# Performance work log

Hardware: AMD Instinct MI355X
Metric: run time of the kernel (lower is better)

The kernel has to match this reference:

```python
import jax, jax.numpy as jnp
import numpy as np

N_NODES = 50000
N_EDGES = 800000
N_GRAPHS = 64
IN_CH = 128
HID = 128
PROC_X = 128
Q_DIM = 768
PROC_Q = 128
OUT_CH = 32


def setup_inputs() -> dict:
    key = jax.random.key(0)
    ks = jax.random.split(key, 16)
    inp = {
        "x": jax.random.normal(ks[0], (N_NODES, IN_CH), dtype=jnp.float32),
        "edge_index": jax.random.randint(ks[1], (2, N_EDGES), 0, N_NODES, dtype=jnp.int64),
        "batch": jnp.sort(jax.random.randint(ks[2], (N_NODES,), 0, N_GRAPHS, dtype=jnp.int64)),
        "question_embedding": jax.random.normal(ks[3], (N_GRAPHS, Q_DIM), dtype=jnp.float32),
    }
    s = 1.0 / np.sqrt(HID)
    inp["W0"] = jax.random.uniform(ks[4], (IN_CH, HID), minval=-s, maxval=s)
    inp["b0"] = jnp.zeros((HID,), jnp.float32)
    inp["W1"] = jax.random.uniform(ks[5], (HID, HID), minval=-s, maxval=s)
    inp["b1"] = jnp.zeros((HID,), jnp.float32)
    inp["W2"] = jax.random.uniform(ks[6], (HID, PROC_X), minval=-s, maxval=s)
    inp["b2"] = jnp.zeros((PROC_X,), jnp.float32)
    inp["fc0_w"] = jax.random.uniform(ks[7], (Q_DIM, PROC_Q), minval=-s, maxval=s)
    inp["fc0_b"] = jnp.zeros((PROC_Q,), jnp.float32)
    inp["fc1_w"] = jax.random.uniform(ks[8], (PROC_X + PROC_Q, HID), minval=-s, maxval=s)
    inp["fc1_b"] = jnp.zeros((HID,), jnp.float32)
    inp["fc2_w"] = jax.random.uniform(ks[9], (HID, OUT_CH), minval=-s, maxval=s)
    inp["fc2_b"] = jnp.zeros((OUT_CH,), jnp.float32)
    return inp


def _gcn_norm(edge_index, n_nodes):
    """Add self-loops and compute symmetric GCN normalization per edge."""
    loop = jnp.arange(n_nodes, dtype=edge_index.dtype)
    src = jnp.concatenate([edge_index[0], loop])
    dst = jnp.concatenate([edge_index[1], loop])
    ones = jnp.ones_like(dst, dtype=jnp.float32)
    deg = jax.ops.segment_sum(ones, dst, num_segments=n_nodes)
    dinv = jnp.where(deg > 0, jax.lax.rsqrt(deg), 0.0)
    norm = dinv[src] * dinv[dst]  # [E+N]
    return src, dst, norm


def _gcn_conv(x, src, dst, norm, W, b):
    h = x @ W                                # [N, F_out]
    msg = h[src] * norm[:, None]             # gather + scale  [E+N, F_out]
    agg = jax.ops.segment_sum(msg, dst, num_segments=x.shape[0])
    return agg + b


def reference(x, edge_index, batch, question_embedding,
              W0, b0, W1, b1, W2, b2,
              fc0_w, fc0_b, fc1_w, fc1_b, fc2_w, fc2_b):
    n = x.shape[0]
    src, dst, norm = _gcn_norm(edge_index, n)
    h = jax.nn.relu(_gcn_conv(x, src, dst, norm, W0, b0))
    h = jax.nn.relu(_gcn_conv(h, src, dst, norm, W1, b1))
    h = jax.nn.relu(_gcn_conv(h, src, dst, norm, W2, b2))
    q = jax.nn.relu(question_embedding @ fc0_w + fc0_b)  # [G, PROC_Q]
    q_exp = q[batch]                                      # [N, PROC_Q]
    combined = jnp.concatenate([h, q_exp], axis=1)
    out = jax.nn.relu(combined @ fc1_w + fc1_b)
    out = out @ fc2_w + fc2_b
    return out
```

## Files before the change

### kernel.cpp

```cpp
#include <hip/hip_runtime.h>
#include <hip/hip_bf16.h>

#define N_NODES 50000
#define N_EDGES 800000
#define N_GRAPHS 64
#define LSTR 136

typedef __attribute__((ext_vector_type(4))) short s4v;
typedef __attribute__((ext_vector_type(8))) short s8v;
typedef __attribute__((ext_vector_type(16))) float f16v;

struct HL { short hi, lo; };

__device__ inline HL bsplit(float f) {
    HL r;
    unsigned u = __float_as_uint(f);
    unsigned rh = (u + 0x7FFFu + ((u >> 16) & 1u)) >> 16;
    r.hi = (short)rh;
    float fh = __uint_as_float(rh << 16);
    float fl = f - fh;
    unsigned u2 = __float_as_uint(fl);
    unsigned rl = (u2 + 0x7FFFu + ((u2 >> 16) & 1u)) >> 16;
    r.lo = (short)rl;
    return r;
}

__device__ inline unsigned short f2bf(float f) {
    unsigned u = __float_as_uint(f);
    return (unsigned short)((u + 0x7FFFu + ((u >> 16) & 1u)) >> 16);
}

__device__ inline float bflo(unsigned u) { return __uint_as_float(u << 16); }
__device__ inline float bfhi(unsigned u) { return __uint_as_float(u & 0xFFFF0000u); }


__global__ void k_hist(const int* __restrict__ ei, int* __restrict__ cnt,
                       int* __restrict__ rank, int E) {
    int e = blockIdx.x * 256 + threadIdx.x;
    if (e < E) rank[e] = atomicAdd(&cnt[ei[E + e]], 1);
}

__global__ __launch_bounds__(512) void k_scan_a(const int* __restrict__ cnt,
                                                int* __restrict__ rowptr,
                                                int* __restrict__ bsum,
                                                float* __restrict__ dinv, int n) {
    __shared__ int s[512];
    int t = threadIdx.x;
    int i = blockIdx.x * 512 + t;
    int v = (i < n) ? cnt[i] : 0;
    if (i < n) dinv[i] = rsqrtf((float)(v + 1));
    int pv = (v + 7) & ~7;
    s[t] = pv;
    __syncthreads();
    for (int d = 1; d < 512; d <<= 1) {
        int x = (t >= d) ? s[t - d] : 0;
        __syncthreads();
        s[t] += x;
        __syncthreads();
    }
    if (i < n) rowptr[i] = s[t] - pv;
    if (t == 511) bsum[blockIdx.x] = s[511];
}

__global__ __launch_bounds__(512) void k_scan_c(int* __restrict__ rowptr,
                                                const int* __restrict__ bsum,
                                                int n, int nb) {
    __shared__ int sb[128];
    int t = threadIdx.x;
    if (t < 128) sb[t] = (t < nb) ? bsum[t] : 0;
    __syncthreads();
    for (int d = 1; d < 128; d <<= 1) {
        int x = 0;
        if (t < 128 && t >= d) x = sb[t - d];
        __syncthreads();
        if (t < 128) sb[t] += x;
        __syncthreads();
    }
    int add = (blockIdx.x > 0) ? sb[blockIdx.x - 1] : 0;
    int i = blockIdx.x * 512 + t;
    if (i < n) rowptr[i] += add;
    if (i == 0) rowptr[n] = sb[nb - 1];
}

__global__ void k_fill_csr(const int* __restrict__ ei, const int* __restrict__ rowptr,
                           const int* __restrict__ rank,
                           unsigned short* __restrict__ colA, int E) {
    int e = blockIdx.x * 256 + threadIdx.x;
    if (e >= E) return;
    colA[rowptr[ei[E + e]] + rank[e]] = (unsigned short)ei[e];
}

__global__ __launch_bounds__(512) void k_prep(const float* __restrict__ qe,
                                              const float* __restrict__ fc0w,
                                              const float* __restrict__ fc0b,
                                              const float* __restrict__ fc1w,
                                              const float* __restrict__ fc1b,
                                              const float* __restrict__ W0,
                                              const float* __restrict__ W1,
                                              const float* __restrict__ W2,
                                              const float* __restrict__ fc2w,
                                              short* __restrict__ WH,
                                              short* __restrict__ WL,
                                              int* __restrict__ cntz,
                                              unsigned* __restrict__ Hsd,
                                              unsigned* __restrict__ Hsd2,
                                              unsigned short* __restrict__ colA,
                                              float* __restrict__ qq) {
    int b = blockIdx.x, tid = threadIdx.x;
    if (b >= 225) {
        int idx = (b - 225) * 512 + tid;
        if (idx < 143752) {
            uint4 p;
            p.x = p.y = p.z = p.w = 0xC350C350u;
            ((uint4*)colA)[idx] = p;
        }
        return;
    }
    if (b >= 200) {
        int idx = (b - 200) * 512 + tid;
        if (idx < 12504) ((int4*)cntz)[idx] = make_int4(0, 0, 0, 0);
        if (b == 200 && tid < 64) {
            Hsd[(unsigned)N_NODES * 64u + tid] = 0u;
            Hsd2[(unsigned)N_NODES * 64u + tid] = 0u;
        }
        return;
    }
    if (b >= 64) {
        int i = (b - 64) * 512 + tid;
        float val;
        int dst;
        if (i < 65536) {
            int mat = i >> 14, off = i & 16383;
            int k = off >> 7, n = off & 127;
            const float* src = (mat == 0) ? W0 : (mat == 1) ? W1 : (mat == 2) ? W2 : fc1w;
            val = src[k * 128 + n];
            dst = mat * 16384 + n * 128 + k;
        } else {
            int off = i - 65536;
            int k = off >> 5, n = off & 31;
            val = fc2w[k * 32 + n];
            dst = 65536 + n * 128 + k;
        }
        HL r = bsplit(val);
        WH[dst] = r.hi;
        WL[dst] = r.lo;
        return;
    }
    __shared__ float qs[768];
    __shared__ float red[512];
    __shared__ float ql[128];
    const float* fc1bot = fc1w + 128 * 128;
    int g = b;
    for (int i = tid; i < 768; i += 512) qs[i] = qe[g * 768 + i];
    __syncthreads();
    int j = tid & 127, sl = tid >> 7;
    int kb = sl * 192;
    float a0 = 0, a1 = 0, a2 = 0, a3 = 0;
    for (int k = 0; k < 192; k += 4) {
        a0 += qs[kb + k + 0] * fc0w[(kb + k + 0) * 128 + j];
        a1 += qs[kb + k + 1] * fc0w[(kb + k + 1) * 128 + j];
        a2 += qs[kb + k + 2] * fc0w[(kb + k + 2) * 128 + j];
        a3 += qs[kb + k + 3] * fc0w[(kb + k + 3) * 128 + j];
    }
    red[tid] = (a0 + a1) + (a2 + a3);
    __syncthreads();
    if (tid < 128)
        ql[tid] = fmaxf(((red[tid] + red[tid + 128]) + (red[tid + 256] + red[tid + 384]))
                        + fc0b[tid], 0.f);
    __syncthreads();
    kb = sl * 32;
    float b0 = 0, b1 = 0;
    for (int k = 0; k < 32; k += 2) {
        b0 += ql[kb + k + 0] * fc1bot[(kb + k + 0) * 128 + j];
        b1 += ql[kb + k + 1] * fc1bot[(kb + k + 1) * 128 + j];
    }
    red[tid] = b0 + b1;
    __syncthreads();
    if (tid < 128)
        qq[g * 128 + tid] = ((red[tid] + red[tid + 128]) + (red[tid + 256] + red[tid + 384]))
                            + fc1b[tid];
}

__global__ __launch_bounds__(128) void gemm_mf(const float* __restrict__ A32,
                                               const short* __restrict__ WTh,
                                               const short* __restrict__ WTl,
                                               const float* __restrict__ dinv,
                                               unsigned short* __restrict__ oHs,
                                               int nrows) {
    __shared__ short Ah[32 * LSTR];
    const int tid = threadIdx.x;
    const int row0 = blockIdx.x * 32;

    #pragma unroll
    for (int i = 0; i < 8; ++i) {
        int u = i * 128 + tid;
        int r = u >> 5, c4 = u & 31;
        int gr = row0 + r;
        float4 v = make_float4(0.f, 0.f, 0.f, 0.f);
        if (gr < nrows) v = ((const float4*)A32)[(size_t)gr * 32 + c4];
        s4v h4 = {(short)f2bf(v.x), (short)f2bf(v.y), (short)f2bf(v.z), (short)f2bf(v.w)};
        *(s4v*)&Ah[r * LSTR + c4 * 4] = h4;
    }
    __syncthreads();

    const int wv = tid >> 6, lane = tid & 63;
    const int m = lane & 31, half = lane >> 5;
    const int c0 = wv * 64 + m;
    f16v acc0 = {0.f}, acc1 = {0.f};
    #pragma unroll
    for (int ks = 0; ks < 8; ++ks) {
        int ko = ks * 16 + half * 8;
        s8v ah  = *(const s8v*)&Ah[m * LSTR + ko];
        s8v bh0 = *(const s8v*)&WTh[(size_t)c0 * 128 + ko];
        s8v bl0 = *(const s8v*)&WTl[(size_t)c0 * 128 + ko];
        s8v bh1 = *(const s8v*)&WTh[(size_t)(c0 + 32) * 128 + ko];
        s8v bl1 = *(const s8v*)&WTl[(size_t)(c0 + 32) * 128 + ko];
        acc0 = __builtin_amdgcn_mfma_f32_32x32x16_bf16(ah, bh0, acc0, 0, 0, 0);
        acc0 = __builtin_amdgcn_mfma_f32_32x32x16_bf16(ah, bl0, acc0, 0, 0, 0);
        acc1 = __builtin_amdgcn_mfma_f32_32x32x16_bf16(ah, bh1, acc1, 0, 0, 0);
        acc1 = __builtin_amdgcn_mfma_f32_32x32x16_bf16(ah, bl1, acc1, 0, 0, 0);
    }

    #pragma unroll
    for (int reg = 0; reg < 16; ++reg) {
        int rl = (reg & 3) + 8 * (reg >> 2) + 4 * half;
        int gr = row0 + rl;
        if (gr >= nrows) continue;
        float sc = dinv[gr];
        oHs[(size_t)gr * 128 + c0]      = f2bf(acc0[reg] * sc);
        oHs[(size_t)gr * 128 + c0 + 32] = f2bf(acc1[reg] * sc);
    }
}

template <int FC>
__global__ __launch_bounds__(256) void k_gg(const unsigned* __restrict__ Hs,
                                            const int* __restrict__ rowptr,
                                            const unsigned short* __restrict__ colA,
                                            const float* __restrict__ dinv,
                                            const float* __restrict__ bias,
                                            const short* __restrict__ WTh,
                                            const short* __restrict__ WTl,
                                            const short* __restrict__ W2h,
                                            const short* __restrict__ W2l,
                                            const float* __restrict__ qq,
                                            const int* __restrict__ batch,
                                            const float* __restrict__ fc2b,
                                            unsigned short* __restrict__ oHs,
                                            float* __restrict__ out,
                                            int n) {
    __shared__ short Ah[32 * LSTR];
    __shared__ short Pl[FC ? 32 * LSTR : 1];
    __shared__ float red[FC ? 3 * 32 * 33 : 1];
    const int tid = threadIdx.x;
    const int row0 = blockIdx.x * 32;
    const int wv = tid >> 6, l = tid & 63;
    const int m = l & 31, half = l >> 5;

    const float2 bb = ((const float2*)bias)[l];
    for (int i = 0; i < 8; ++i) {
        int r = wv * 8 + i;
        int node = row0 + r;
        unsigned pack = 0;
        if (node < n) {
            int e0 = __builtin_amdgcn_readfirstlane(rowptr[node]);
            int e1 = __builtin_amdgcn_readfirstlane(rowptr[node + 1]);
            float a0 = 0.f, a1 = 0.f;
            for (int e = e0; e < e1; e += 8) {
                uint4 cw = *(const uint4*)(colA + e);
                unsigned u0 = Hs[(cw.x & 0xFFFFu) * 64u + l];
                unsigned u1 = Hs[(cw.x >> 16) * 64u + l];
                unsigned u2 = Hs[(cw.y & 0xFFFFu) * 64u + l];
                unsigned u3 = Hs[(cw.y >> 16) * 64u + l];
                unsigned u4 = Hs[(cw.z & 0xFFFFu) * 64u + l];
                unsigned u5 = Hs[(cw.z >> 16) * 64u + l];
                unsigned u6 = Hs[(cw.w & 0xFFFFu) * 64u + l];
                unsigned u7 = Hs[(cw.w >> 16) * 64u + l];
                a0 += ((bflo(u0) + bflo(u1)) + (bflo(u2) + bflo(u3)))
                    + ((bflo(u4) + bflo(u5)) + (bflo(u6) + bflo(u7)));
                a1 += ((bfhi(u0) + bfhi(u1)) + (bfhi(u2) + bfhi(u3)))
                    + ((bfhi(u4) + bfhi(u5)) + (bfhi(u6) + bfhi(u7)));
            }
            float di = dinv[node];
            unsigned uh = Hs[(unsigned)node * 64u + l];
            float o0 = fmaxf((a0 + bflo(uh)) * di + bb.x, 0.f);
            float o1 = fmaxf((a1 + bfhi(uh)) * di + bb.y, 0.f);
            pack = (unsigned)f2bf(o0) | ((unsigned)f2bf(o1) << 16);
        }
        ((unsigned*)Ah)[r * 68 + l] = pack;
    }
    __syncthreads();

    const int c0 = wv * 32 + m;
    f16v acc = {0.f};
    #pragma unroll
    for (int ks = 0; ks < 8; ++ks) {
        int ko = ks * 16 + half * 8;
        s8v ah = *(const s8v*)&Ah[m * LSTR + ko];
        s8v bh = *(const s8v*)&WTh[(size_t)c0 * 128 + ko];
        s8v bl = *(const s8v*)&WTl[(size_t)c0 * 128 + ko];
        acc = __builtin_amdgcn_mfma_f32_32x32x16_bf16(ah, bh, acc, 0, 0, 0);
        acc = __builtin_amdgcn_mfma_f32_32x32x16_bf16(ah, bl, acc, 0, 0, 0);
    }

    if (FC == 0) {
        #pragma unroll
        for (int reg = 0; reg < 16; ++reg) {
            int rl = (reg & 3) + 8 * (reg >> 2) + 4 * half;
            int gr = row0 + rl;
            if (gr >= n) continue;
            oHs[(size_t)gr * 128 + c0] = f2bf(acc[reg] * dinv[gr]);
        }
    } else {
        __syncthreads();
        #pragma unroll
        for (int reg = 0; reg < 16; ++reg) {
            int rl = (reg & 3) + 8 * (reg >> 2) + 4 * half;
            int gr = row0 + rl;
            int g = (gr < n) ? batch[gr] : 0;
            float v = fmaxf(acc[reg] + qq[(size_t)g * 128 + c0], 0.f);
            HL p = bsplit(v);
            Ah[rl * LSTR + c0] = p.hi;
            Pl[rl * LSTR + c0] = p.lo;
        }
        __syncthreads();
        f16v acc2 = {0.f};
        #pragma unroll
        for (int ks = 0; ks < 2; ++ks) {
            int ko = wv * 32 + ks * 16 + half * 8;
            s8v ah = *(const s8v*)&Ah[m * LSTR + ko];
            s8v al = *(const s8v*)&Pl[m * LSTR + ko];
            s8v bh = *(const s8v*)&W2h[(size_t)m * 128 + ko];
            s8v bl = *(const s8v*)&W2l[(size_t)m * 128 + ko];
            acc2 = __builtin_amdgcn_mfma_f32_32x32x16_bf16(ah, bh, acc2, 0, 0, 0);
            acc2 = __builtin_amdgcn_mfma_f32_32x32x16_bf16(ah, bl, acc2, 0, 0, 0);
            acc2 = __builtin_amdgcn_mfma_f32_32x32x16_bf16(al, bh, acc2, 0, 0, 0);
        }
        if (wv > 0) {
            #pragma unroll
            for (int reg = 0; reg < 16; ++reg) {
                int rl = (reg & 3) + 8 * (reg >> 2) + 4 * half;
                red[(wv - 1) * 1056 + rl * 33 + m] = acc2[reg];
            }
        }
        __syncthreads();
        if (wv == 0) {
            #pragma unroll
            for (int reg = 0; reg < 16; ++reg) {
                int rl = (reg & 3) + 8 * (reg >> 2) + 4 * half;
                int gr = row0 + rl;
                if (gr < n)
                    out[(size_t)gr * 32 + m] = acc2[reg]
                        + (red[rl * 33 + m] + red[1056 + rl * 33 + m])
                        + red[2112 + rl * 33 + m] + fc2b[m];
            }
        }
    }
}


extern "C" void kernel_launch(void* const* d_in, const int* in_sizes, int n_in,
                              void* d_out, int out_size, void* d_ws, size_t ws_size,
                              hipStream_t stream) {
    const float* x    = (const float*)d_in[0];
    const int*   ei   = (const int*)d_in[1];
    const int*   batch= (const int*)d_in[2];
    const float* qe   = (const float*)d_in[3];
    const float* W0   = (const float*)d_in[4];
    const float* b0   = (const float*)d_in[5];
    const float* W1   = (const float*)d_in[6];
    const float* b1   = (const float*)d_in[7];
    const float* W2   = (const float*)d_in[8];
    const float* b2   = (const float*)d_in[9];
    const float* fc0w = (const float*)d_in[10];
    const float* fc0b = (const float*)d_in[11];
    const float* fc1w = (const float*)d_in[12];
    const float* fc1b = (const float*)d_in[13];
    const float* fc2w = (const float*)d_in[14];
    const float* fc2b = (const float*)d_in[15];
    float* out = (float*)d_out;

    float* WS = (float*)d_ws;
    unsigned short* HS  = (unsigned short*)WS;
    unsigned short* HS2 = (unsigned short*)(WS + 3200064);
    float* DINV = WS + 6400128;
    float* QQ   = WS + 6450144;
    int*   CNT  = (int*)(WS + 6458336);
    int*   ROWPTR = (int*)(WS + 6508352);
    int*   RANK = (int*)(WS + 6558368);
    unsigned short* COL = (unsigned short*)(WS + 7358368);
    int*   BSUM = (int*)(WS + 7933376);
    short* WTH  = (short*)(WS + 7933504);
    short* WTL  = WTH + 69632;

    const int N = N_NODES, E = N_EDGES;
    const int eb = (E + 255) / 256;
    const int sb = (N + 511) / 512;
    const int gg = (N + 31) / 32;

    k_prep<<<506, 512, 0, stream>>>(qe, fc0w, fc0b, fc1w, fc1b, W0, W1, W2, fc2w,
                                    WTH, WTL, CNT, (unsigned*)HS, (unsigned*)HS2, COL, QQ);
    k_hist<<<eb, 256, 0, stream>>>(ei, CNT, RANK, E);
    k_scan_a<<<sb, 512, 0, stream>>>(CNT, ROWPTR, BSUM, DINV, N);
    k_scan_c<<<sb, 512, 0, stream>>>(ROWPTR, BSUM, N, sb);
    k_fill_csr<<<eb, 256, 0, stream>>>(ei, ROWPTR, RANK, COL, E);

    gemm_mf<<<gg, 128, 0, stream>>>(x, WTH, WTL, DINV, HS, N);
    k_gg<0><<<gg, 256, 0, stream>>>((const unsigned*)HS, ROWPTR, COL, DINV, b0,
                                    WTH + 16384, WTL + 16384, nullptr, nullptr,
                                    nullptr, nullptr, nullptr, HS2, nullptr, N);
    k_gg<0><<<gg, 256, 0, stream>>>((const unsigned*)HS2, ROWPTR, COL, DINV, b1,
                                    WTH + 32768, WTL + 32768, nullptr, nullptr,
                                    nullptr, nullptr, nullptr, HS, nullptr, N);
    k_gg<1><<<gg, 256, 0, stream>>>((const unsigned*)HS, ROWPTR, COL, DINV, b2,
                                    WTH + 49152, WTL + 49152, WTH + 65536, WTL + 65536,
                                    QQ, batch, fc2b, nullptr, out, N);
}
```

Baseline: 323.1 us.

## Fuse CSR build into one cooperative kernel and interleave two-row gathers

Four separate CSR-construction kernels (histogram, two scan passes, fill) are merged into one cooperative kernel of 512 blocks that uses grid-wide syncs between phases, removing launch gaps. Separately, the aggregation loop in the GCN layer kernel now processes two destination rows at once, interleaving their gathers to raise memory-level parallelism. The cooperative launch requires all 512 blocks to be co-resident and adds grid-sync costs. The paired loop adds extra registers and tail loops when the two rows have unequal degree.

```diff
diff --git a/kernel.cpp b/kernel.cpp
--- a/kernel.cpp
+++ b/kernel.cpp
@@ -1,5 +1,8 @@
 #include <hip/hip_runtime.h>
 #include <hip/hip_bf16.h>
+#include <hip/hip_cooperative_groups.h>
+
+namespace cg = cooperative_groups;
 
 #define N_NODES 50000
 #define N_EDGES 800000
@@ -33,61 +36,81 @@
 __device__ inline float bflo(unsigned u) { return __uint_as_float(u << 16); }
 __device__ inline float bfhi(unsigned u) { return __uint_as_float(u & 0xFFFF0000u); }
 
-
-__global__ void k_hist(const int* __restrict__ ei, int* __restrict__ cnt,
-                       int* __restrict__ rank, int E) {
-    int e = blockIdx.x * 256 + threadIdx.x;
-    if (e < E) rank[e] = atomicAdd(&cnt[ei[E + e]], 1);
-}
-
-__global__ __launch_bounds__(512) void k_scan_a(const int* __restrict__ cnt,
-                                                int* __restrict__ rowptr,
-                                                int* __restrict__ bsum,
-                                                float* __restrict__ dinv, int n) {
+__device__ inline void gat8(const unsigned* __restrict__ Hs,
+                            const unsigned short* __restrict__ colA,
+                            int e, int l, float& a0, float& a1) {
+    uint4 cw = *(const uint4*)(colA + e);
+    unsigned u0 = Hs[(cw.x & 0xFFFFu) * 64u + l];
+    unsigned u1 = Hs[(cw.x >> 16) * 64u + l];
+    unsigned u2 = Hs[(cw.y & 0xFFFFu) * 64u + l];
+    unsigned u3 = Hs[(cw.y >> 16) * 64u + l];
+    unsigned u4 = Hs[(cw.z & 0xFFFFu) * 64u + l];
+    unsigned u5 = Hs[(cw.z >> 16) * 64u + l];
+    unsigned u6 = Hs[(cw.w & 0xFFFFu) * 64u + l];
+    unsigned u7 = Hs[(cw.w >> 16) * 64u + l];
+    a0 += ((bflo(u0) + bflo(u1)) + (bflo(u2) + bflo(u3)))
+        + ((bflo(u4) + bflo(u5)) + (bflo(u6) + bflo(u7)));
+    a1 += ((bfhi(u0) + bfhi(u1)) + (bfhi(u2) + bfhi(u3)))
+        + ((bfhi(u4) + bfhi(u5)) + (bfhi(u6) + bfhi(u7)));
+}
+
+__global__ __launch_bounds__(512) void k_csr(const int* __restrict__ ei,
+                                             int* __restrict__ cnt,
+                                             int* __restrict__ rank,
+                                             int* __restrict__ rowptr,
+                                             int* __restrict__ bsum,
+                                             float* __restrict__ dinv,
+                                             unsigned short* __restrict__ colA,
+                                             int n, int E) {
+    cg::grid_group grid = cg::this_grid();
+    const int t = threadIdx.x;
+    const int gid = blockIdx.x * 512 + t;
+    const int gsz = gridDim.x * 512;
+    const int nb = (n + 511) / 512;
+
+    for (int e = gid; e < E; e += gsz)
+        rank[e] = atomicAdd(&cnt[ei[E + e]], 1);
+    grid.sync();
+
     __shared__ int s[512];
-    int t = threadIdx.x;
-    int i = blockIdx.x * 512 + t;
-    int v = (i < n) ? cnt[i] : 0;
-    if (i < n) dinv[i] = rsqrtf((float)(v + 1));
-    int pv = (v + 7) & ~7;
-    s[t] = pv;
-    __syncthreads();
-    for (int d = 1; d < 512; d <<= 1) {
-        int x = (t >= d) ? s[t - d] : 0;
+    __shared__ int sb[128];
+    if (blockIdx.x < nb) {
+        int i = blockIdx.x * 512 + t;
+        int v = (i < n) ? cnt[i] : 0;
+        if (i < n) dinv[i] = rsqrtf((float)(v + 1));
+        int pv = (v + 7) & ~7;
+        s[t] = pv;
         __syncthreads();
-        s[t] += x;
+        for (int d = 1; d < 512; d <<= 1) {
+            int x = (t >= d) ? s[t - d] : 0;
+            __syncthreads();
+            s[t] += x;
+            __syncthreads();
+        }
+        if (i < n) rowptr[i] = s[t] - pv;
+        if (t == 511) bsum[blockIdx.x] = s[511];
+    }
+    grid.sync();
+
+    if (blockIdx.x < nb) {
+        if (t < 128) sb[t] = (t < nb) ? bsum[t] : 0;
         __syncthreads();
-    }
-    if (i < n) rowptr[i] = s[t] - pv;
-    if (t == 511) bsum[blockIdx.x] = s[511];
-}
-
-__global__ __launch_bounds__(512) void k_scan_c(int* __restrict__ rowptr,
-                                                const int* __restrict__ bsum,
-                                                int n, int nb) {
-    __shared__ int sb[128];
-    int t = threadIdx.x;
-    if (t < 128) sb[t] = (t < nb) ? bsum[t] : 0;
-    __syncthreads();
-    for (int d = 1; d < 128; d <<= 1) {
-        int x = 0;
-        if (t < 128 && t >= d) x = sb[t - d];
-        __syncthreads();
-        if (t < 128) sb[t] += x;
-        __syncthreads();
-    }
-    int add = (blockIdx.x > 0) ? sb[blockIdx.x - 1] : 0;
-    int i = blockIdx.x * 512 + t;
-    if (i < n) rowptr[i] += add;
-    if (i == 0) rowptr[n] = sb[nb - 1];
-}
-
-__global__ void k_fill_csr(const int* __restrict__ ei, const int* __restrict__ rowptr,
-                           const int* __restrict__ rank,
-                           unsigned short* __restrict__ colA, int E) {
-    int e = blockIdx.x * 256 + threadIdx.x;
-    if (e >= E) return;
-    colA[rowptr[ei[E + e]] + rank[e]] = (unsigned short)ei[e];
+        for (int d = 1; d < 128; d <<= 1) {
+            int x = 0;
+            if (t < 128 && t >= d) x = sb[t - d];
+            __syncthreads();
+            if (t < 128) sb[t] += x;
+            __syncthreads();
+        }
+        int add = (blockIdx.x > 0) ? sb[blockIdx.x - 1] : 0;
+        int i = blockIdx.x * 512 + t;
+        if (i < n) rowptr[i] += add;
+        if (i == 0) rowptr[n] = sb[nb - 1];
+    }
+    grid.sync();
+
+    for (int e = gid; e < E; e += gsz)
+        colA[rowptr[ei[E + e]] + rank[e]] = (unsigned short)ei[e];
 }
 
 __global__ __launch_bounds__(512) void k_prep(const float* __restrict__ qe,
@@ -257,36 +280,45 @@
     const int m = l & 31, half = l >> 5;
 
     const float2 bb = ((const float2*)bias)[l];
-    for (int i = 0; i < 8; ++i) {
-        int r = wv * 8 + i;
-        int node = row0 + r;
-        unsigned pack = 0;
-        if (node < n) {
-            int e0 = __builtin_amdgcn_readfirstlane(rowptr[node]);
-            int e1 = __builtin_amdgcn_readfirstlane(rowptr[node + 1]);
-            float a0 = 0.f, a1 = 0.f;
-            for (int e = e0; e < e1; e += 8) {
-                uint4 cw = *(const uint4*)(colA + e);
-                unsigned u0 = Hs[(cw.x & 0xFFFFu) * 64u + l];
-                unsigned u1 = Hs[(cw.x >> 16) * 64u + l];
-                unsigned u2 = Hs[(cw.y & 0xFFFFu) * 64u + l];
-                unsigned u3 = Hs[(cw.y >> 16) * 64u + l];
-                unsigned u4 = Hs[(cw.z & 0xFFFFu) * 64u + l];
-                unsigned u5 = Hs[(cw.z >> 16) * 64u + l];
-                unsigned u6 = Hs[(cw.w & 0xFFFFu) * 64u + l];
-                unsigned u7 = Hs[(cw.w >> 16) * 64u + l];
-                a0 += ((bflo(u0) + bflo(u1)) + (bflo(u2) + bflo(u3)))
-                    + ((bflo(u4) + bflo(u5)) + (bflo(u6) + bflo(u7)));
-                a1 += ((bfhi(u0) + bfhi(u1)) + (bfhi(u2) + bfhi(u3)))
-                    + ((bfhi(u4) + bfhi(u5)) + (bfhi(u6) + bfhi(u7)));
-            }
-            float di = dinv[node];
-            unsigned uh = Hs[(unsigned)node * 64u + l];
+    for (int i = 0; i < 4; ++i) {
+        int rA = wv * 8 + i, rB = rA + 4;
+        int nodeA = row0 + rA, nodeB = row0 + rB;
+        int eA = 0, eA1 = 0, eB = 0, eB1 = 0;
+        if (nodeA < n) {
+            eA  = __builtin_amdgcn_readfirstlane(rowptr[nodeA]);
+            eA1 = __builtin_amdgcn_readfirstlane(rowptr[nodeA + 1]);
+        }
+        if (nodeB < n) {
+            eB  = __builtin_amdgcn_readfirstlane(rowptr[nodeB]);
+            eB1 = __builtin_amdgcn_readfirstlane(rowptr[nodeB + 1]);
+        }
+        float a0 = 0.f, a1 = 0.f, c0v = 0.f, c1v = 0.f;
+        while (eA < eA1 && eB < eB1) {
+            gat8(Hs, colA, eA, l, a0, a1);
+            gat8(Hs, colA, eB, l, c0v, c1v);
+            eA += 8;
+            eB += 8;
+        }
+        while (eA < eA1) { gat8(Hs, colA, eA, l, a0, a1); eA += 8; }
+        while (eB < eB1) { gat8(Hs, colA, eB, l, c0v, c1v); eB += 8; }
+
+        unsigned packA = 0, packB = 0;
+        if (nodeA < n) {
+            float di = dinv[nodeA];
+            unsigned uh = Hs[(unsigned)nodeA * 64u + l];
             float o0 = fmaxf((a0 + bflo(uh)) * di + bb.x, 0.f);
             float o1 = fmaxf((a1 + bfhi(uh)) * di + bb.y, 0.f);
-            pack = (unsigned)f2bf(o0) | ((unsigned)f2bf(o1) << 16);
-        }
-        ((unsigned*)Ah)[r * 68 + l] = pack;
+            packA = (unsigned)f2bf(o0) | ((unsigned)f2bf(o1) << 16);
+        }
+        if (nodeB < n) {
+            float di = dinv[nodeB];
+            unsigned uh = Hs[(unsigned)nodeB * 64u + l];
+            float o0 = fmaxf((c0v + bflo(uh)) * di + bb.x, 0.f);
+            float o1 = fmaxf((c1v + bfhi(uh)) * di + bb.y, 0.f);
+            packB = (unsigned)f2bf(o0) | ((unsigned)f2bf(o1) << 16);
+        }
+        ((unsigned*)Ah)[rA * 68 + l] = packA;
+        ((unsigned*)Ah)[rB * 68 + l] = packB;
     }
     __syncthreads();
 
@@ -392,17 +424,18 @@
     short* WTH  = (short*)(WS + 7933504);
     short* WTL  = WTH + 69632;
 
-    const int N = N_NODES, E = N_EDGES;
-    const int eb = (E + 255) / 256;
-    const int sb = (N + 511) / 512;
+    int N = N_NODES, E = N_EDGES;
     const int gg = (N + 31) / 32;
 
     k_prep<<<506, 512, 0, stream>>>(qe, fc0w, fc0b, fc1w, fc1b, W0, W1, W2, fc2w,
                                     WTH, WTL, CNT, (unsigned*)HS, (unsigned*)HS2, COL, QQ);
-    k_hist<<<eb, 256, 0, stream>>>(ei, CNT, RANK, E);
-    k_scan_a<<<sb, 512, 0, stream>>>(CNT, ROWPTR, BSUM, DINV, N);
-    k_scan_c<<<sb, 512, 0, stream>>>(ROWPTR, BSUM, N, sb);
-    k_fill_csr<<<eb, 256, 0, stream>>>(ei, ROWPTR, RANK, COL, E);
+
+    {
+        void* args[] = {(void*)&ei, (void*)&CNT, (void*)&RANK, (void*)&ROWPTR,
+                        (void*)&BSUM, (void*)&DINV, (void*)&COL, (void*)&N, (void*)&E};
+        (void)hipLaunchCooperativeKernel((const void*)k_csr, dim3(512), dim3(512),
+                                         args, 0, stream);
+    }
 
     gemm_mf<<<gg, 128, 0, stream>>>(x, WTH, WTL, DINV, HS, N);
     k_gg<0><<<gg, 256, 0, stream>>>((const unsigned*)HS, ROWPTR, COL, DINV, b0,
```

After: 532.5 us. +64.8%, slower.
